# Performance work log

Hardware: AMD Instinct MI355X
Metric: run time of the kernel (lower is better)

## Reference

```python
import jax, jax.numpy as jnp
import numpy as np

N = 50000
IN_F = 128
OUT_F = 128
NRELA = 128
E1 = 400000
E2 = 100000
ALPHA = 0.2   # LeakyReLU slope
D = 0.85      # PageRank damping
EPS = 1e-12


def setup_inputs() -> dict:
    key = jax.random.key(0)
    ks = jax.random.split(key, 8)
    return {
        "input": jax.random.normal(ks[0], (N, IN_F), dtype=jnp.float32),
        "edge": jax.random.randint(ks[1], (2, E1), 0, N, dtype=jnp.int64),
        "edge_embed": jax.random.normal(ks[2], (E1, NRELA), dtype=jnp.float32),
        "edge_list_nhop": jax.random.randint(ks[3], (2, E2), 0, N, dtype=jnp.int64),
        "edge_embed_nhop": jax.random.normal(ks[4], (E2, NRELA), dtype=jnp.float32),
        "entity_rank": jax.random.uniform(ks[5], (N,), dtype=jnp.float32),
        "a": 0.05 * jax.random.normal(ks[6], (OUT_F, 2 * IN_F + NRELA), dtype=jnp.float32),
        "a_2": 0.05 * jax.random.normal(ks[7], (1, OUT_F), dtype=jnp.float32),
    }


def reference(input, edge, edge_embed, edge_list_nhop, edge_embed_nhop, entity_rank, a, a_2):
    n = input.shape[0]
    # concat n-hop edges (len(edge_list_nhop) != 0 path in the original)
    e = jnp.concatenate([edge, edge_list_nhop], axis=1)          # [2, E]
    emb = jnp.concatenate([edge_embed, edge_embed_nhop], axis=0) # [E, nrela]
    src, dst = e[0], e[1]

    # edge MLP: edge_h = [x_src | x_dst | rel]  -> a @ edge_h^T, leakyrelu
    edge_h = jnp.concatenate([input[src], input[dst], emb], axis=1)   # [E, 2*in+nrela]
    edge_m = jax.nn.leaky_relu(edge_h @ a.T, ALPHA)                   # [E, out]
    powers = -jax.nn.leaky_relu(edge_m @ a_2[0], ALPHA)               # [E]
    edge_e = jnp.exp(powers)                                          # [E]

    # softmax-like normalization over incoming edges of each target node
    a_rowsum = jax.ops.segment_sum(edge_e, dst, num_segments=n)       # [N]
    a_rowsum = jnp.where(a_rowsum == 0.0, EPS, a_rowsum)
    rel_att = edge_e / a_rowsum[dst]                                  # [E]

    # PageRank-style rank update
    e_rowsum = jax.ops.segment_sum(rel_att, src, num_segments=n)      # [N] (out-sum)
    e_rowsum = jnp.where(e_rowsum == 0.0, EPS, e_rowsum)
    val = rel_att * entity_rank[src] / e_rowsum[src]                  # [E]
    e_colsum = jax.ops.segment_sum(val, dst, num_segments=n)          # [N]
    new_rank = 1.0 - D + D * e_colsum                                 # [N]

    # rank-weighted attention propagation of edge features
    edge_prop = (rel_att * new_rank[src])[:, None] * edge_m           # [E, out]
    h_prime = jax.ops.segment_sum(edge_prop, dst, num_segments=n)     # [N, out]

    return jax.nn.elu(h_prime), new_rank
```

## Files before the change

### kernel.cpp

```cpp
#include <hip/hip_runtime.h>
#include <math.h>

#define N_NODES 50000
#define E1N 400000
#define E2N 100000
#define E_TOT 500000
#define ALPHAC 0.2f
#define DAMP 0.85f
#define EPSC 1e-12f

typedef __bf16 bf16_t;
typedef __bf16 bf16x4 __attribute__((ext_vector_type(4)));
typedef __bf16 bf16x8 __attribute__((ext_vector_type(8)));
typedef float f32x16 __attribute__((ext_vector_type(16)));

__device__ __forceinline__ float lrelu(float x) { return x > 0.f ? x : ALPHAC * x; }

__global__ __launch_bounds__(256) void k_pack12(const float* __restrict__ a,
                                                bf16_t* __restrict__ bp) {
  int i = blockIdx.x * 256 + threadIdx.x;
  if (i >= 32768) return;
  int j = i & 7;
  int l = (i >> 3) & 63;
  int nt = (i >> 9) & 7;
  int ks = i >> 12;
  int c = nt * 32 + (l & 31);
  int o = (c < 128) ? c : c - 128;
  int koff = (c < 128) ? 0 : 128;
  int k = ks * 16 + ((l >> 5) << 3) + j;
  bp[i] = (bf16_t)a[o * 384 + koff + k];
}

__global__ __launch_bounds__(256) void k_pack3(const float* __restrict__ a,
                                               bf16_t* __restrict__ bp) {
  int i = blockIdx.x * 256 + threadIdx.x;
  if (i >= 16384) return;
  int j = i & 7;
  int l = (i >> 3) & 63;
  int nt = (i >> 9) & 3;
  int ks = i >> 11;
  int o = nt * 32 + (l & 31);
  int k = ks * 16 + ((l >> 5) << 3) + j;
  bp[i] = (bf16_t)a[o * 384 + 256 + k];
}

__global__ __launch_bounds__(256) void k_edges(const int* __restrict__ edge,
                                               const int* __restrict__ nhop,
                                               int* __restrict__ sidx,
                                               int* __restrict__ didx, int stride) {
  int e = blockIdx.x * 256 + threadIdx.x;
  if (e >= E_TOT) return;
  if (e < E1N) {
    sidx[e] = edge[(size_t)e * stride];
    didx[e] = edge[(size_t)(E1N + e) * stride];
  } else {
    int t = e - E1N;
    sidx[e] = nhop[(size_t)t * stride];
    didx[e] = nhop[(size_t)(E2N + t) * stride];
  }
}

__global__ __launch_bounds__(256) void k_uv(const float* __restrict__ input,
                                            const bf16_t* __restrict__ bp12,
                                            bf16_t* __restrict__ uv) {
  const int tid = threadIdx.x, lane = tid & 63, wv = tid >> 6;
  const int n0 = blockIdx.x * 128 + wv * 32;
  const int m = lane & 31, hi2 = lane >> 5;
  int n = n0 + m;
  if (n >= N_NODES) n = 0;
  const float* ar = input + (size_t)n * 128 + hi2 * 8;
  const bf16x8* bp = (const bf16x8*)bp12;

  f32x16 acc[8];
#pragma unroll
  for (int nt = 0; nt < 8; ++nt)
#pragma unroll
    for (int r = 0; r < 16; ++r) acc[nt][r] = 0.f;

#pragma unroll
  for (int ks = 0; ks < 8; ++ks) {
    float4 u0 = *(const float4*)(ar + ks * 16);
    float4 u1 = *(const float4*)(ar + ks * 16 + 4);
    bf16x8 af = {(bf16_t)u0.x, (bf16_t)u0.y, (bf16_t)u0.z, (bf16_t)u0.w,
                 (bf16_t)u1.x, (bf16_t)u1.y, (bf16_t)u1.z, (bf16_t)u1.w};
#pragma unroll
    for (int nt = 0; nt < 8; ++nt)
      acc[nt] = __builtin_amdgcn_mfma_f32_32x32x16_bf16(af, bp[(ks * 8 + nt) * 64 + lane],
                                                        acc[nt], 0, 0, 0);
  }
#pragma unroll
  for (int nt = 0; nt < 8; ++nt)
#pragma unroll
    for (int r = 0; r < 16; ++r) {
      int row = (r & 3) + ((r >> 2) << 3) + (hi2 << 2);
      int node = n0 + row;
      if (node < N_NODES) uv[(size_t)node * 256 + nt * 32 + m] = (bf16_t)acc[nt][r];
    }
}

template <bool ACCUM>
__global__ __launch_bounds__(256, 3) void k_pass(
    const float* __restrict__ eemb, const float* __restrict__ eembn,
    const bf16_t* __restrict__ uv, const int* __restrict__ sidx,
    const int* __restrict__ didx, const bf16_t* __restrict__ bp3,
    const float* __restrict__ a2, float* __restrict__ edge_e,
    float* __restrict__ a_rowsum, const float* __restrict__ rel_att,
    const float* __restrict__ new_rank, float* __restrict__ hout) {
  __shared__ bf16_t s_sum[128][136];
  const int tid = threadIdx.x;
  const long long e0 = (long long)blockIdx.x * 128;

  {
    const int g = tid >> 5;
    const int cl = (tid & 31) * 4;
#pragma unroll
    for (int i = 0; i < 16; ++i) {
      int el = i * 8 + g;
      long long e = e0 + el;
      float sx = 0.f, sy = 0.f, sz = 0.f, sw = 0.f;
      if (e < E_TOT) {
        int s = sidx[e], d = didx[e];
        bf16x4 u = *(const bf16x4*)(uv + (size_t)s * 256 + cl);
        bf16x4 v = *(const bf16x4*)(uv + (size_t)d * 256 + 128 + cl);
        sx = (float)u[0] + (float)v[0];
        sy = (float)u[1] + (float)v[1];
        sz = (float)u[2] + (float)v[2];
        sw = (float)u[3] + (float)v[3];
      }
      bf16x4 o = {(bf16_t)sx, (bf16_t)sy, (bf16_t)sz, (bf16_t)sw};
      *(bf16x4*)&s_sum[el][cl] = o;
    }
  }
  __syncthreads();

  const int lane = tid & 63;
  const int wv = tid >> 6;
  const long long e0w = e0 + wv * 32;
  if (e0w >= E_TOT) return;
  const int m = lane & 31, hi2 = lane >> 5;
  const long long e = e0w + m;
  const float* b2 = (e < E1N) ? (eemb + (size_t)e * 128)
                              : (eembn + (size_t)(e - E1N) * 128);
  const float* ar = b2 + hi2 * 8;

  const bf16x8* bp = (const bf16x8*)bp3;
  f32x16 acc[4];
#pragma unroll
  for (int nt = 0; nt < 4; ++nt)
#pragma unroll
    for (int r = 0; r < 16; ++r) acc[nt][r] = 0.f;

  auto loadA = [&](int ks) -> bf16x8 {
    float4 u0 = *(const float4*)(ar + ks * 16);
    float4 u1 = *(const float4*)(ar + ks * 16 + 4);
    bf16x8 rr = {(bf16_t)u0.x, (bf16_t)u0.y, (bf16_t)u0.z, (bf16_t)u0.w,
                 (bf16_t)u1.x, (bf16_t)u1.y, (bf16_t)u1.z, (bf16_t)u1.w};
    return rr;
  };

  bf16x8 a_cur = loadA(0);
  bf16x8 bb[4], bn[4];
#pragma unroll
  for (int nt = 0; nt < 4; ++nt) bb[nt] = bp[nt * 64 + lane];

#pragma unroll
  for (int ks = 0; ks < 8; ++ks) {
    bf16x8 a_nxt;
    if (ks < 7) {
      a_nxt = loadA(ks + 1);
#pragma unroll
      for (int nt = 0; nt < 4; ++nt) bn[nt] = bp[((ks + 1) * 4 + nt) * 64 + lane];
    }
#pragma unroll
    for (int nt = 0; nt < 4; ++nt)
      acc[nt] = __builtin_amdgcn_mfma_f32_32x32x16_bf16(a_cur, bb[nt], acc[nt], 0, 0, 0);
    a_cur = a_nxt;
#pragma unroll
    for (int nt = 0; nt < 4; ++nt) bb[nt] = bn[nt];
  }

  if (!ACCUM) {
    float sac[16];
#pragma unroll
    for (int r = 0; r < 16; ++r) sac[r] = 0.f;
#pragma unroll
    for (int nt = 0; nt < 4; ++nt) {
      float a2v = a2[nt * 32 + m];
      int o = nt * 32 + m;
#pragma unroll
      for (int r = 0; r < 16; ++r) {
        int row = (r & 3) + ((r >> 2) << 3) + (hi2 << 2);
        float c = acc[nt][r] + (float)s_sum[wv * 32 + row][o];
        sac[r] += lrelu(c) * a2v;
      }
    }
#pragma unroll
    for (int off = 1; off < 32; off <<= 1) {
#pragma unroll
      for (int r = 0; r < 16; ++r) sac[r] += __shfl_xor(sac[r], off, 64);
    }
    if (m == 0) {
#pragma unroll
      for (int r = 0; r < 16; ++r) {
        int row = (r & 3) + ((r >> 2) << 3) + (hi2 << 2);
        long long ee_i = e0w + row;
        float ev = expf(-lrelu(sac[r]));
        edge_e[ee_i] = ev;
        atomicAdd(&a_rowsum[didx[ee_i]], ev);
      }
    }
  } else {
    float w_m = rel_att[e] * new_rank[sidx[e]];
    int d = didx[e];
    float wr[16];
    int dr[16];
#pragma unroll
    for (int r = 0; r < 16; ++r) {
      int row = (r & 3) + ((r >> 2) << 3) + (hi2 << 2);
      wr[r] = __shfl(w_m, row, 64);
      dr[r] = __shfl(d, row, 64);
    }
#pragma unroll
    for (int nt = 0; nt < 4; ++nt) {
      int o = nt * 32 + m;
#pragma unroll
      for (int r = 0; r < 16; ++r) {
        int row = (r & 3) + ((r >> 2) << 3) + (hi2 << 2);
        float c = acc[nt][r] + (float)s_sum[wv * 32 + row][o];
        atomicAdd(&hout[(size_t)dr[r] * 128 + o], lrelu(c) * wr[r]);
      }
    }
  }
}

__global__ __launch_bounds__(256) void k_relatt(const float* __restrict__ edge_e,
                                                const int* __restrict__ didx,
                                                const int* __restrict__ sidx,
                                                const float* __restrict__ a_rowsum,
                                                float* __restrict__ rel_att,
                                                float* __restrict__ e_rowsum) {
  int e = blockIdx.x * 256 + threadIdx.x;
  if (e >= E_TOT) return;
  float rs = a_rowsum[didx[e]];
  rs = (rs == 0.f) ? EPSC : rs;
  float r = edge_e[e] / rs;
  rel_att[e] = r;
  atomicAdd(&e_rowsum[sidx[e]], r);
}

__global__ __launch_bounds__(256) void k_val(const float* __restrict__ rel_att,
                                             const int* __restrict__ sidx,
                                             const int* __restrict__ didx,
                                             const float* __restrict__ rank,
                                             const float* __restrict__ e_rowsum,
                                             float* __restrict__ e_colsum) {
  int e = blockIdx.x * 256 + threadIdx.x;
  if (e >= E_TOT) return;
  int s = sidx[e];
  float er = e_rowsum[s];
  er = (er == 0.f) ? EPSC : er;
  float val = rel_att[e] * rank[s] / er;
  atomicAdd(&e_colsum[didx[e]], val);
}

__global__ __launch_bounds__(256) void k_rank(const float* __restrict__ e_colsum,
                                              float* __restrict__ new_rank,
                                              float* __restrict__ out_tail) {
  int n = blockIdx.x * 256 + threadIdx.x;
  if (n >= N_NODES) return;
  float nr = 1.f - DAMP + DAMP * e_colsum[n];
  new_rank[n] = nr;
  out_tail[n] = nr;
}

__global__ __launch_bounds__(256) void k_elu(float* __restrict__ h) {
  int i = blockIdx.x * 256 + threadIdx.x;
  if (i < N_NODES * 128) {
    float x = h[i];
    h[i] = x > 0.f ? x : expm1f(x);
  }
}

extern "C" void kernel_launch(void* const* d_in, const int* in_sizes, int n_in,
                              void* d_out, int out_size, void* d_ws, size_t ws_size,
                              hipStream_t stream) {
  const float* input = (const float*)d_in[0];
  const int* edge = (const int*)d_in[1];
  const float* eemb = (const float*)d_in[2];
  const int* enh = (const int*)d_in[3];
  const float* eembn = (const float*)d_in[4];
  const float* rank = (const float*)d_in[5];
  const float* a = (const float*)d_in[6];
  const float* a2 = (const float*)d_in[7];
  float* out = (float*)d_out;

  int estride = (in_sizes[1] == 2 * E1N) ? 1 : 2;

  char* ws = (char*)d_ws;
  bf16_t* bp12 = (bf16_t*)(ws);
  bf16_t* bp3 = (bf16_t*)(ws + 65536);
  bf16_t* uv = (bf16_t*)(ws + 98304);
  int* sidx = (int*)(ws + 25698304);
  int* didx = (int*)(ws + 27698304);
  float* edge_e = (float*)(ws + 29698304);
  float* rel_att = (float*)(ws + 31698304);
  float* a_rowsum = (float*)(ws + 33698304);
  float* e_rowsum = (float*)(ws + 33898304);
  float* e_colsum = (float*)(ws + 34098304);
  float* new_rank = (float*)(ws + 34298304);

  hipMemsetAsync(a_rowsum, 0, 3 * 200000, stream);
  hipMemsetAsync(out, 0, (size_t)N_NODES * 128 * 4, stream);

  k_pack12<<<128, 256, 0, stream>>>(a, bp12);
  k_pack3<<<64, 256, 0, stream>>>(a, bp3);
  k_edges<<<(E_TOT + 255) / 256, 256, 0, stream>>>(edge, enh, sidx, didx, estride);
  k_uv<<<(N_NODES + 127) / 128, 256, 0, stream>>>(input, bp12, uv);

  const int NB = (E_TOT + 127) / 128;
  const int EB = (E_TOT + 255) / 256;
  k_pass<false><<<NB, 256, 0, stream>>>(eemb, eembn, uv, sidx, didx, bp3, a2,
                                        edge_e, a_rowsum, nullptr, nullptr, nullptr);
  k_relatt<<<EB, 256, 0, stream>>>(edge_e, didx, sidx, a_rowsum, rel_att, e_rowsum);
  k_val<<<EB, 256, 0, stream>>>(rel_att, sidx, didx, rank, e_rowsum, e_colsum);
  k_rank<<<(N_NODES + 255) / 256, 256, 0, stream>>>(e_colsum, new_rank,
                                                    out + (size_t)N_NODES * 128);
  k_pass<true><<<NB, 256, 0, stream>>>(eemb, eembn, uv, sidx, didx, bp3, a2,
                                       nullptr, nullptr, rel_att, new_rank, out);
  k_elu<<<(N_NODES * 128 + 255) / 256, 256, 0, stream>>>(out);
}
```

Measured before the change: 789.4 us.

## Store edge_m once and gather h_prime by destination CSR instead of atomics

Pass A now writes the LeakyReLU'd edge features to a large bf16 workspace buffer P. It also builds a destination-sorted CSR (counts, a single-block scan, atomic-cursor positions). A new per-node kernel gathers each node's incoming edges, weights them by rel_att*new_rank, and applies ELU inline. This removes the second edge GEMM pass, about 64M float atomics into the output, the output memset and the separate ELU kernel. In exchange it writes and re-reads a 128 MB intermediate, and the new path runs only when the workspace is big enough; otherwise the old path is used.

```diff
diff --git a/kernel.cpp b/kernel.cpp
--- a/kernel.cpp
+++ b/kernel.cpp
@@ -47,17 +47,56 @@
 __global__ __launch_bounds__(256) void k_edges(const int* __restrict__ edge,
                                                const int* __restrict__ nhop,
                                                int* __restrict__ sidx,
-                                               int* __restrict__ didx, int stride) {
+                                               int* __restrict__ didx, int stride,
+                                               int* __restrict__ cnt) {
   int e = blockIdx.x * 256 + threadIdx.x;
   if (e >= E_TOT) return;
+  int s, d;
   if (e < E1N) {
-    sidx[e] = edge[(size_t)e * stride];
-    didx[e] = edge[(size_t)(E1N + e) * stride];
+    s = edge[(size_t)e * stride];
+    d = edge[(size_t)(E1N + e) * stride];
   } else {
     int t = e - E1N;
-    sidx[e] = nhop[(size_t)t * stride];
-    didx[e] = nhop[(size_t)(E2N + t) * stride];
-  }
+    s = nhop[(size_t)t * stride];
+    d = nhop[(size_t)(E2N + t) * stride];
+  }
+  sidx[e] = s;
+  didx[e] = d;
+  if (cnt) atomicAdd(&cnt[d], 1);
+}
+
+__global__ __launch_bounds__(256) void k_scan(const int* __restrict__ cnt,
+                                              int* __restrict__ csr_start,
+                                              int* __restrict__ cursor) {
+  __shared__ int ls[256];
+  __shared__ int lofs[256];
+  int t = threadIdx.x;
+  int lo = t * 196, hi = lo + 196;
+  if (hi > N_NODES) hi = N_NODES;
+  int s = 0;
+  for (int i = lo; i < hi; ++i) s += cnt[i];
+  ls[t] = s;
+  __syncthreads();
+  if (t == 0) {
+    int run = 0;
+    for (int i = 0; i < 256; ++i) { lofs[i] = run; run += ls[i]; }
+  }
+  __syncthreads();
+  int run = lofs[t];
+  for (int i = lo; i < hi; ++i) {
+    csr_start[i] = run;
+    cursor[i] = run;
+    run += cnt[i];
+  }
+}
+
+__global__ __launch_bounds__(256) void k_pos(const int* __restrict__ didx,
+                                             int* __restrict__ cursor,
+                                             int* __restrict__ eid) {
+  int e = blockIdx.x * 256 + threadIdx.x;
+  if (e >= E_TOT) return;
+  int pos = atomicAdd(&cursor[didx[e]], 1);
+  eid[pos] = e;
 }
 
 __global__ __launch_bounds__(256) void k_uv(const float* __restrict__ input,
@@ -98,14 +137,12 @@
     }
 }
 
-template <bool ACCUM>
-__global__ __launch_bounds__(256, 3) void k_pass(
+__global__ __launch_bounds__(256, 3) void k_passA(
     const float* __restrict__ eemb, const float* __restrict__ eembn,
     const bf16_t* __restrict__ uv, const int* __restrict__ sidx,
     const int* __restrict__ didx, const bf16_t* __restrict__ bp3,
     const float* __restrict__ a2, float* __restrict__ edge_e,
-    float* __restrict__ a_rowsum, const float* __restrict__ rel_att,
-    const float* __restrict__ new_rank, float* __restrict__ hout) {
+    float* __restrict__ a_rowsum, bf16_t* __restrict__ P) {
   __shared__ bf16_t s_sum[128][136];
   const int tid = threadIdx.x;
   const long long e0 = (long long)blockIdx.x * 128;
@@ -179,6 +216,150 @@
     for (int nt = 0; nt < 4; ++nt) bb[nt] = bn[nt];
   }
 
+  bf16_t* Pt = P + ((long long)blockIdx.x * 4 + wv) * 4096;
+  float sac[16];
+#pragma unroll
+  for (int r = 0; r < 16; ++r) sac[r] = 0.f;
+#pragma unroll
+  for (int nt = 0; nt < 4; ++nt) {
+    int o = nt * 32 + m;
+    float a2v = a2[o];
+#pragma unroll
+    for (int r = 0; r < 16; ++r) {
+      int row = (r & 3) + ((r >> 2) << 3) + (hi2 << 2);
+      float c = acc[nt][r] + (float)s_sum[wv * 32 + row][o];
+      float p = lrelu(c);
+      Pt[(nt * 16 + r) * 64 + lane] = (bf16_t)p;
+      sac[r] += p * a2v;
+    }
+  }
+#pragma unroll
+  for (int off = 1; off < 32; off <<= 1) {
+#pragma unroll
+    for (int r = 0; r < 16; ++r) sac[r] += __shfl_xor(sac[r], off, 64);
+  }
+  if (m == 0) {
+#pragma unroll
+    for (int r = 0; r < 16; ++r) {
+      int row = (r & 3) + ((r >> 2) << 3) + (hi2 << 2);
+      long long ee_i = e0w + row;
+      float ev = expf(-lrelu(sac[r]));
+      edge_e[ee_i] = ev;
+      atomicAdd(&a_rowsum[didx[ee_i]], ev);
+    }
+  }
+}
+
+__global__ __launch_bounds__(256) void k_hprime(const bf16_t* __restrict__ P,
+                                                const int* __restrict__ eid,
+                                                const int* __restrict__ csr_start,
+                                                const int* __restrict__ cnt,
+                                                const float* __restrict__ w,
+                                                float* __restrict__ out) {
+  int g = (blockIdx.x << 3) | (threadIdx.x >> 5);
+  if (g >= N_NODES) return;
+  int m = threadIdx.x & 31;
+  int start = csr_start[g], deg = cnt[g];
+  float a0 = 0.f, a1 = 0.f, a2v = 0.f, a3v = 0.f;
+  for (int i = 0; i < deg; ++i) {
+    int e = eid[start + i];
+    float we = w[e];
+    int row = e & 31;
+    int r = (row & 3) | ((row >> 3) << 2);
+    int hi2 = (row >> 2) & 1;
+    const bf16_t* p = P + (long long)(e >> 5) * 4096 + r * 64 + hi2 * 32 + m;
+    a0 += we * (float)p[0];
+    a1 += we * (float)p[16 * 64];
+    a2v += we * (float)p[32 * 64];
+    a3v += we * (float)p[48 * 64];
+  }
+  float* o = out + (size_t)g * 128 + m;
+  o[0] = a0 > 0.f ? a0 : expm1f(a0);
+  o[32] = a1 > 0.f ? a1 : expm1f(a1);
+  o[64] = a2v > 0.f ? a2v : expm1f(a2v);
+  o[96] = a3v > 0.f ? a3v : expm1f(a3v);
+}
+
+template <bool ACCUM>
+__global__ __launch_bounds__(256, 3) void k_pass(
+    const float* __restrict__ eemb, const float* __restrict__ eembn,
+    const bf16_t* __restrict__ uv, const int* __restrict__ sidx,
+    const int* __restrict__ didx, const bf16_t* __restrict__ bp3,
+    const float* __restrict__ a2, float* __restrict__ edge_e,
+    float* __restrict__ a_rowsum, const float* __restrict__ rel_att,
+    const float* __restrict__ new_rank, float* __restrict__ hout) {
+  __shared__ bf16_t s_sum[128][136];
+  const int tid = threadIdx.x;
+  const long long e0 = (long long)blockIdx.x * 128;
+  {
+    const int g = tid >> 5;
+    const int cl = (tid & 31) * 4;
+#pragma unroll
+    for (int i = 0; i < 16; ++i) {
+      int el = i * 8 + g;
+      long long e = e0 + el;
+      float sx = 0.f, sy = 0.f, sz = 0.f, sw = 0.f;
+      if (e < E_TOT) {
+        int s = sidx[e], d = didx[e];
+        bf16x4 u = *(const bf16x4*)(uv + (size_t)s * 256 + cl);
+        bf16x4 v = *(const bf16x4*)(uv + (size_t)d * 256 + 128 + cl);
+        sx = (float)u[0] + (float)v[0];
+        sy = (float)u[1] + (float)v[1];
+        sz = (float)u[2] + (float)v[2];
+        sw = (float)u[3] + (float)v[3];
+      }
+      bf16x4 o = {(bf16_t)sx, (bf16_t)sy, (bf16_t)sz, (bf16_t)sw};
+      *(bf16x4*)&s_sum[el][cl] = o;
+    }
+  }
+  __syncthreads();
+
+  const int lane = tid & 63;
+  const int wv = tid >> 6;
+  const long long e0w = e0 + wv * 32;
+  if (e0w >= E_TOT) return;
+  const int m = lane & 31, hi2 = lane >> 5;
+  const long long e = e0w + m;
+  const float* b2 = (e < E1N) ? (eemb + (size_t)e * 128)
+                              : (eembn + (size_t)(e - E1N) * 128);
+  const float* ar = b2 + hi2 * 8;
+
+  const bf16x8* bp = (const bf16x8*)bp3;
+  f32x16 acc[4];
+#pragma unroll
+  for (int nt = 0; nt < 4; ++nt)
+#pragma unroll
+    for (int r = 0; r < 16; ++r) acc[nt][r] = 0.f;
+
+  auto loadA = [&](int ks) -> bf16x8 {
+    float4 u0 = *(const float4*)(ar + ks * 16);
+    float4 u1 = *(const float4*)(ar + ks * 16 + 4);
+    bf16x8 rr = {(bf16_t)u0.x, (bf16_t)u0.y, (bf16_t)u0.z, (bf16_t)u0.w,
+                 (bf16_t)u1.x, (bf16_t)u1.y, (bf16_t)u1.z, (bf16_t)u1.w};
+    return rr;
+  };
+
+  bf16x8 a_cur = loadA(0);
+  bf16x8 bb[4], bn[4];
+#pragma unroll
+  for (int nt = 0; nt < 4; ++nt) bb[nt] = bp[nt * 64 + lane];
+
+#pragma unroll
+  for (int ks = 0; ks < 8; ++ks) {
+    bf16x8 a_nxt;
+    if (ks < 7) {
+      a_nxt = loadA(ks + 1);
+#pragma unroll
+      for (int nt = 0; nt < 4; ++nt) bn[nt] = bp[((ks + 1) * 4 + nt) * 64 + lane];
+    }
+#pragma unroll
+    for (int nt = 0; nt < 4; ++nt)
+      acc[nt] = __builtin_amdgcn_mfma_f32_32x32x16_bf16(a_cur, bb[nt], acc[nt], 0, 0, 0);
+    a_cur = a_nxt;
+#pragma unroll
+    for (int nt = 0; nt < 4; ++nt) bb[nt] = bn[nt];
+  }
+
   if (!ACCUM) {
     float sac[16];
 #pragma unroll
@@ -273,6 +454,14 @@
   out_tail[n] = nr;
 }
 
+__global__ __launch_bounds__(256) void k_w(const float* __restrict__ rel_att,
+                                           const int* __restrict__ sidx,
+                                           const float* __restrict__ new_rank,
+                                           float* __restrict__ w) {
+  int e = blockIdx.x * 256 + threadIdx.x;
+  if (e < E_TOT) w[e] = rel_att[e] * new_rank[sidx[e]];
+}
+
 __global__ __launch_bounds__(256) void k_elu(float* __restrict__ h) {
   int i = blockIdx.x * 256 + threadIdx.x;
   if (i < N_NODES * 128) {
@@ -304,28 +493,57 @@
   int* didx = (int*)(ws + 27698304);
   float* edge_e = (float*)(ws + 29698304);
   float* rel_att = (float*)(ws + 31698304);
-  float* a_rowsum = (float*)(ws + 33698304);
-  float* e_rowsum = (float*)(ws + 33898304);
-  float* e_colsum = (float*)(ws + 34098304);
-  float* new_rank = (float*)(ws + 34298304);
-
-  hipMemsetAsync(a_rowsum, 0, 3 * 200000, stream);
-  hipMemsetAsync(out, 0, (size_t)N_NODES * 128 * 4, stream);
-
-  k_pack12<<<128, 256, 0, stream>>>(a, bp12);
-  k_pack3<<<64, 256, 0, stream>>>(a, bp3);
-  k_edges<<<(E_TOT + 255) / 256, 256, 0, stream>>>(edge, enh, sidx, didx, estride);
-  k_uv<<<(N_NODES + 127) / 128, 256, 0, stream>>>(input, bp12, uv);
+  float* warr = (float*)(ws + 33698304);
+  int* eid = (int*)(ws + 35698304);
+  int* csr_start = (int*)(ws + 37698304);
+  int* cursor = (int*)(ws + 37898304);
+  int* cnt = (int*)(ws + 38098304);
+  float* a_rowsum = (float*)(ws + 38298304);
+  float* e_rowsum = (float*)(ws + 38498304);
+  float* e_colsum = (float*)(ws + 38698304);
+  float* new_rank = (float*)(ws + 38898304);
+  bf16_t* P = (bf16_t*)(ws + 39098304);
+
+  const bool big = ws_size >= 167098304ULL;
 
   const int NB = (E_TOT + 127) / 128;
   const int EB = (E_TOT + 255) / 256;
-  k_pass<false><<<NB, 256, 0, stream>>>(eemb, eembn, uv, sidx, didx, bp3, a2,
-                                        edge_e, a_rowsum, nullptr, nullptr, nullptr);
-  k_relatt<<<EB, 256, 0, stream>>>(edge_e, didx, sidx, a_rowsum, rel_att, e_rowsum);
-  k_val<<<EB, 256, 0, stream>>>(rel_att, sidx, didx, rank, e_rowsum, e_colsum);
-  k_rank<<<(N_NODES + 255) / 256, 256, 0, stream>>>(e_colsum, new_rank,
-                                                    out + (size_t)N_NODES * 128);
-  k_pass<true><<<NB, 256, 0, stream>>>(eemb, eembn, uv, sidx, didx, bp3, a2,
-                                       nullptr, nullptr, rel_att, new_rank, out);
-  k_elu<<<(N_NODES * 128 + 255) / 256, 256, 0, stream>>>(out);
-}
+
+  if (big) {
+    hipMemsetAsync(cnt, 0, 4 * 200000, stream);
+
+    k_pack12<<<128, 256, 0, stream>>>(a, bp12);
+    k_pack3<<<64, 256, 0, stream>>>(a, bp3);
+    k_edges<<<EB, 256, 0, stream>>>(edge, enh, sidx, didx, estride, cnt);
+    k_scan<<<1, 256, 0, stream>>>(cnt, csr_start, cursor);
+    k_pos<<<EB, 256, 0, stream>>>(didx, cursor, eid);
+    k_uv<<<(N_NODES + 127) / 128, 256, 0, stream>>>(input, bp12, uv);
+
+    k_passA<<<NB, 256, 0, stream>>>(eemb, eembn, uv, sidx, didx, bp3, a2,
+                                    edge_e, a_rowsum, P);
+    k_relatt<<<EB, 256, 0, stream>>>(edge_e, didx, sidx, a_rowsum, rel_att, e_rowsum);
+    k_val<<<EB, 256, 0, stream>>>(rel_att, sidx, didx, rank, e_rowsum, e_colsum);
+    k_rank<<<(N_NODES + 255) / 256, 256, 0, stream>>>(e_colsum, new_rank,
+                                                      out + (size_t)N_NODES * 128);
+    k_w<<<EB, 256, 0, stream>>>(rel_att, sidx, new_rank, warr);
+    k_hprime<<<(N_NODES + 7) / 8, 256, 0, stream>>>(P, eid, csr_start, cnt, warr, out);
+  } else {
+    hipMemsetAsync(cnt, 0, 4 * 200000, stream);
+    hipMemsetAsync(out, 0, (size_t)N_NODES * 128 * 4, stream);
+
+    k_pack12<<<128, 256, 0, stream>>>(a, bp12);
+    k_pack3<<<64, 256, 0, stream>>>(a, bp3);
+    k_edges<<<EB, 256, 0, stream>>>(edge, enh, sidx, didx, estride, nullptr);
+    k_uv<<<(N_NODES + 127) / 128, 256, 0, stream>>>(input, bp12, uv);
+
+    k_pass<false><<<NB, 256, 0, stream>>>(eemb, eembn, uv, sidx, didx, bp3, a2,
+                                          edge_e, a_rowsum, nullptr, nullptr, nullptr);
+    k_relatt<<<EB, 256, 0, stream>>>(edge_e, didx, sidx, a_rowsum, rel_att, e_rowsum);
+    k_val<<<EB, 256, 0, stream>>>(rel_att, sidx, didx, rank, e_rowsum, e_colsum);
+    k_rank<<<(N_NODES + 255) / 256, 256, 0, stream>>>(e_colsum, new_rank,
+                                                      out + (size_t)N_NODES * 128);
+    k_pass<true><<<NB, 256, 0, stream>>>(eemb, eembn, uv, sidx, didx, bp3, a2,
+                                         nullptr, nullptr, rel_att, new_rank, out);
+    k_elu<<<(N_NODES * 128 + 255) / 256, 256, 0, stream>>>(out);
+  }
+}
```

Result: faster. 743.5 us (-5.8%).
